# Performance work log

Hardware: AMD Instinct MI355X
Metric: run time of the kernel (lower is better)

## Reference

```python
import jax, jax.numpy as jnp
import numpy as np

N_HARM_XYZ = 6
N_HARM_DIR = 4
HIDDEN_XYZ = 256
HIDDEN_DIR = 128
EMB_XYZ = N_HARM_XYZ * 2 * 3 + 3  # 39
EMB_DIR = N_HARM_DIR * 2 * 3 + 3  # 27


def harmonic_embedding(x, n_harmonics):
    # x: [..., 3] -> [..., n_harmonics*2*3 + 3]
    freqs = 2.0 ** jnp.arange(n_harmonics, dtype=x.dtype)  # logspace, omega0=1
    emb = (x[..., None] * freqs).reshape(*x.shape[:-1], -1)  # [..., 3*n_harm]
    return jnp.concatenate([jnp.sin(emb), jnp.cos(emb), x], axis=-1)


def setup_inputs() -> dict:
    key = jax.random.key(0)
    ks = jax.random.split(key, 32)
    R, P = 2048, 64
    inp = {
        'sample_points': jax.random.normal(ks[0], (R, P, 3), dtype=jnp.float32),
        'directions': jax.random.normal(ks[1], (R, 3), dtype=jnp.float32),
    }
    # trunk layer dims (skip concat before layer 5; last layer outputs hidden+1)
    dims_in = [EMB_XYZ, HIDDEN_XYZ, HIDDEN_XYZ, HIDDEN_XYZ, HIDDEN_XYZ,
               HIDDEN_XYZ + EMB_XYZ, HIDDEN_XYZ, HIDDEN_XYZ]
    dims_out = [HIDDEN_XYZ] * 7 + [HIDDEN_XYZ + 1]
    for i, (di, do) in enumerate(zip(dims_in, dims_out)):
        s = 1.0 / np.sqrt(di)
        inp[f'W{i}'] = jax.random.uniform(ks[2 + 2 * i], (di, do), jnp.float32, -s, s)
        inp[f'b{i}'] = jax.random.uniform(ks[3 + 2 * i], (do,), jnp.float32, -s, s)
    s = 1.0 / np.sqrt(HIDDEN_XYZ + EMB_DIR)
    inp['Wc'] = jax.random.uniform(ks[20], (HIDDEN_XYZ + EMB_DIR, HIDDEN_DIR), jnp.float32, -s, s)
    inp['bc'] = jax.random.uniform(ks[21], (HIDDEN_DIR,), jnp.float32, -s, s)
    s = 1.0 / np.sqrt(HIDDEN_DIR)
    inp['Wo'] = jax.random.uniform(ks[22], (HIDDEN_DIR, 3), jnp.float32, -s, s)
    inp['bo'] = jax.random.uniform(ks[23], (3,), jnp.float32, -s, s)
    return inp


def nerf_forward(sample_points, directions,
                 W0, b0, W1, b1, W2, b2, W3, b3, W4, b4, W5, b5, W6, b6, W7, b7,
                 Wc, bc, Wo, bo):
    R, P, _ = sample_points.shape
    pts = sample_points.reshape(-1, 3)              # [N, 3]
    e = harmonic_embedding(pts, N_HARM_XYZ)         # [N, 39]
    h = e
    # seq0: layers 0-4, ReLU after each
    for W, b in ((W0, b0), (W1, b1), (W2, b2), (W3, b3), (W4, b4)):
        h = jax.nn.relu(h @ W + b)
    # skip concat with xyz embedding, then seq1: layers 5-7 (no ReLU after last)
    h = jnp.concatenate([h, e], axis=-1)            # [N, 295]
    h = jax.nn.relu(h @ W5 + b5)
    h = jax.nn.relu(h @ W6 + b6)
    h = h @ W7 + b7                                  # [N, 257]
    sigma = jax.nn.relu(h[:, 0]).reshape(R, P, 1)
    dirs = jnp.broadcast_to(directions[:, None, :], (R, P, 3)).reshape(-1, 3)
    d = harmonic_embedding(dirs, N_HARM_DIR)         # [N, 27]
    c = jnp.concatenate([h[:, 1:], d], axis=-1)      # [N, 283]
    c = jax.nn.relu(c @ Wc + bc)
    color = jax.nn.sigmoid(c @ Wo + bo).reshape(R, P, 3)
    return color, sigma


def reference(sample_points, directions,
              W0, b0, W1, b1, W2, b2, W3, b3, W4, b4, W5, b5, W6, b6, W7, b7,
              Wc, bc, Wo, bo):
    # returns (feature, density) matching the torch dict values
    return nerf_forward(sample_points, directions,
                        W0, b0, W1, b1, W2, b2, W3, b3, W4, b4, W5, b5, W6, b6, W7, b7,
                        Wc, bc, Wo, bo)
```

## Files before the change

kernel.cpp:

```cpp
#include <hip/hip_runtime.h>

typedef __attribute__((ext_vector_type(8))) __bf16 bf16x8;
typedef __attribute__((ext_vector_type(4))) float float4_;
typedef __attribute__((ext_vector_type(4))) unsigned short ushort4_;

#define ACT_STRIDE 264
#define EMB_STRIDE 72

#define OFF_W0T 0
#define OFF_W1T 16384
#define OFF_W2T 81920
#define OFF_W3T 147456
#define OFF_W4T 212992
#define OFF_W5T 278528
#define OFF_W6T 360448
#define OFF_W7T 425984
#define OFF_WCT 491520
#define BF16_TOTAL 524288
#define WSF_BYTE_OFF (BF16_TOTAL * 2)

__device__ __forceinline__ unsigned short f2b(float v) {
  union { float f; unsigned u; } a; a.f = v;
  unsigned r = a.u + 0x7fffu + ((a.u >> 16) & 1u);
  return (unsigned short)(r >> 16);
}
__device__ __forceinline__ float b2f(unsigned short h) {
  union { unsigned u; float f; } a; a.u = ((unsigned)h) << 16;
  return a.f;
}

__global__ __launch_bounds__(256) void prep_kernel(
    const float* __restrict__ W0, const float* __restrict__ W1,
    const float* __restrict__ W2, const float* __restrict__ W3,
    const float* __restrict__ W4, const float* __restrict__ W5,
    const float* __restrict__ W6, const float* __restrict__ W7,
    const float* __restrict__ Wc, const float* __restrict__ b7,
    unsigned short* __restrict__ wsb, float* __restrict__ wsf)
{
  int i = blockIdx.x * 256 + threadIdx.x;
  const float* src; int rs, K, Kp, n, k2; unsigned short* base;
  if (i < 8192)        { int t = i;          n = t & 255; k2 = t >> 8; src = W0; rs = 256; K = 39;  Kp = 64;  base = wsb + OFF_W0T; }
  else if (i < 139264) { int t = i - 8192;   int l = t >> 15; t &= 32767;
                         n = t & 255; k2 = t >> 8;
                         src = (l == 0) ? W1 : (l == 1) ? W2 : (l == 2) ? W3 : W4;
                         rs = 256; K = 256; Kp = 256; base = wsb + OFF_W1T + l * 65536; }
  else if (i < 180224) { int t = i - 139264; n = t & 255; k2 = t >> 8; src = W5;     rs = 256; K = 295; Kp = 320; base = wsb + OFF_W5T; }
  else if (i < 212992) { int t = i - 180224; n = t & 255; k2 = t >> 8; src = W6;     rs = 256; K = 256; Kp = 256; base = wsb + OFF_W6T; }
  else if (i < 245760) { int t = i - 212992; n = t & 255; k2 = t >> 8; src = W7 + 1; rs = 257; K = 256; Kp = 256; base = wsb + OFF_W7T; }
  else if (i < 262144) { int t = i - 245760; n = t & 127; k2 = t >> 7; src = Wc;     rs = 128; K = 256; Kp = 256; base = wsb + OFF_WCT; }
  else if (i < 262400) { int k = i - 262144; wsf[k] = W7[k * 257]; return; }
  else if (i < 262656) { int k = i - 262400; wsf[256 + k] = b7[k + 1]; return; }
  else return;
  const int k = k2 * 2;
  const float v0 = (k     < K) ? src[k * rs + n]       : 0.f;
  const float v1 = (k + 1 < K) ? src[(k + 1) * rs + n] : 0.f;
  const int off = (((n >> 4) * (Kp >> 5)) + (k >> 5)) * 512
                + ((k >> 3) & 3) * 128 + (n & 15) * 8 + (k & 7);
  const unsigned val = (unsigned)f2b(v0) | ((unsigned)f2b(v1) << 16);
  *(unsigned*)(base + off) = val;
}

template<bool RELU>
__device__ __forceinline__ void layer_mm(
    const unsigned short* src1, int stride1, int ks1,
    const unsigned short* src2, int stride2, int ks2,
    const unsigned short* __restrict__ wT, int kTiles,
    const float* bias, unsigned short* dst, int lane, int wave)
{
  const int c = lane & 15, q = lane >> 4;
  const int nt0 = wave * 2, n0 = wave * 32;
  float4_ acc[4][2] = {};

#pragma unroll
  for (int ks = 0; ks < 8; ++ks) {
    if (ks >= ks1) break;
    bf16x8 bfr[4];
    const unsigned short* p = src1 + c * stride1 + ks * 32 + q * 8;
#pragma unroll
    for (int mi = 0; mi < 4; ++mi)
      bfr[mi] = *(const bf16x8*)(p + mi * 16 * stride1);
#pragma unroll
    for (int ni = 0; ni < 2; ++ni) {
      bf16x8 afr = *(const bf16x8*)(wT + ((nt0 + ni) * kTiles + ks) * 512 + lane * 8);
#pragma unroll
      for (int mi = 0; mi < 4; ++mi)
        acc[mi][ni] = __builtin_amdgcn_mfma_f32_16x16x32_bf16(afr, bfr[mi], acc[mi][ni], 0, 0, 0);
    }
  }
#pragma unroll
  for (int ks = 0; ks < 2; ++ks) {
    if (ks >= ks2) break;
    bf16x8 bfr[4];
    const unsigned short* p = src2 + c * stride2 + ks * 32 + q * 8;
#pragma unroll
    for (int mi = 0; mi < 4; ++mi)
      bfr[mi] = *(const bf16x8*)(p + mi * 16 * stride2);
#pragma unroll
    for (int ni = 0; ni < 2; ++ni) {
      bf16x8 afr = *(const bf16x8*)(wT + ((nt0 + ni) * kTiles + ks1 + ks) * 512 + lane * 8);
#pragma unroll
      for (int mi = 0; mi < 4; ++mi)
        acc[mi][ni] = __builtin_amdgcn_mfma_f32_16x16x32_bf16(afr, bfr[mi], acc[mi][ni], 0, 0, 0);
    }
  }
#pragma unroll
  for (int ni = 0; ni < 2; ++ni) {
    const int n = n0 + ni * 16 + q * 4;
    float4_ bv = *(const float4_*)(bias + n);
#pragma unroll
    for (int mi = 0; mi < 4; ++mi) {
      float4_ v = acc[mi][ni] + bv;
      if (RELU) {
        v.x = fmaxf(v.x, 0.f); v.y = fmaxf(v.y, 0.f);
        v.z = fmaxf(v.z, 0.f); v.w = fmaxf(v.w, 0.f);
      }
      ushort4_ pk = { f2b(v.x), f2b(v.y), f2b(v.z), f2b(v.w) };
      *(ushort4_*)(dst + (mi * 16 + c) * ACT_STRIDE + n) = pk;
    }
  }
}

__global__ __launch_bounds__(512, 4) void nerf_kernel(
    const float* __restrict__ pts, const float* __restrict__ dirs,
    const float* __restrict__ b0, const float* __restrict__ b1,
    const float* __restrict__ b2, const float* __restrict__ b3,
    const float* __restrict__ b4, const float* __restrict__ b5,
    const float* __restrict__ b6, const float* __restrict__ b7,
    const float* __restrict__ Wc, const float* __restrict__ bc,
    const float* __restrict__ Wo, const float* __restrict__ bo,
    const unsigned short* __restrict__ wsb, const float* __restrict__ wsf,
    float* __restrict__ out)
{
  __shared__ __align__(16) unsigned short sA[64 * ACT_STRIDE];
  __shared__ __align__(16) unsigned short sB[64 * ACT_STRIDE];
  __shared__ __align__(16) unsigned short sE[64 * EMB_STRIDE];
  __shared__ float s_dvec[27];
  __shared__ float s_biasc[128];

  const int ray = blockIdx.x;
  const int t = threadIdx.x;
  const int lane = t & 63;
  const int wave = t >> 6;

  {
    const int m = t >> 3, s8 = t & 7;
    const float* pb = pts + (ray * 64 + m) * 3;
    const float x0 = pb[0], x1 = pb[1], x2 = pb[2];
#pragma unroll
    for (int j = 0; j < 9; ++j) {
      const int cc = s8 * 9 + j;
      float v = 0.f;
      if (cc < 18) {
        const float xx = (cc < 6) ? x0 : (cc < 12) ? x1 : x2;
        v = sinf(xx * (float)(1 << (cc % 6)));
      } else if (cc < 36) {
        const int c2 = cc - 18;
        const float xx = (c2 < 6) ? x0 : (c2 < 12) ? x1 : x2;
        v = cosf(xx * (float)(1 << (c2 % 6)));
      } else if (cc == 36) v = x0;
      else if (cc == 37) v = x1;
      else if (cc == 38) v = x2;
      sE[m * EMB_STRIDE + cc] = f2b(v);
    }
  }
  if (t < 27) {
    const float* db = dirs + ray * 3;
    float v;
    if (t < 12) v = sinf(db[t >> 2] * (float)(1 << (t & 3)));
    else if (t < 24) { const int j = t - 12; v = cosf(db[j >> 2] * (float)(1 << (j & 3))); }
    else v = db[t - 24];
    s_dvec[t] = v;
  }
  __syncthreads();
  if (t < 128) {
    float s = bc[t];
#pragma unroll
    for (int j = 0; j < 27; ++j) s += s_dvec[j] * Wc[(256 + j) * 128 + t];
    s_biasc[t] = s;
  }

  layer_mm<true >(sE, EMB_STRIDE, 2, nullptr, 0, 0, wsb + OFF_W0T, 2,  b0, sA, lane, wave); __syncthreads();
  layer_mm<true >(sA, ACT_STRIDE, 8, nullptr, 0, 0, wsb + OFF_W1T, 8,  b1, sB, lane, wave); __syncthreads();
  layer_mm<true >(sB, ACT_STRIDE, 8, nullptr, 0, 0, wsb + OFF_W2T, 8,  b2, sA, lane, wave); __syncthreads();
  layer_mm<true >(sA, ACT_STRIDE, 8, nullptr, 0, 0, wsb + OFF_W3T, 8,  b3, sB, lane, wave); __syncthreads();
  layer_mm<true >(sB, ACT_STRIDE, 8, nullptr, 0, 0, wsb + OFF_W4T, 8,  b4, sA, lane, wave); __syncthreads();
  layer_mm<true >(sA, ACT_STRIDE, 8, sE, EMB_STRIDE, 2, wsb + OFF_W5T, 10, b5, sB, lane, wave); __syncthreads();
  layer_mm<true >(sB, ACT_STRIDE, 8, nullptr, 0, 0, wsb + OFF_W6T, 8,  b6, sA, lane, wave); __syncthreads();

  {
    const int m = t >> 3, q8 = t & 7;
    const unsigned short* p = sA + m * ACT_STRIDE + q8 * 32;
    const float* w = wsf + q8 * 32;
    float s = 0.f;
#pragma unroll
    for (int i = 0; i < 4; ++i) {
      bf16x8 hv = *(const bf16x8*)(p + i * 8);
#pragma unroll
      for (int j = 0; j < 8; ++j) s += (float)hv[j] * w[i * 8 + j];
    }
    s += __shfl_xor(s, 1); s += __shfl_xor(s, 2); s += __shfl_xor(s, 4);
    if (q8 == 0) out[393216 + ray * 64 + m] = fmaxf(s + b7[0], 0.f);
  }

  layer_mm<false>(sA, ACT_STRIDE, 8, nullptr, 0, 0, wsb + OFF_W7T, 8, wsf + 256, sB, lane, wave); __syncthreads();
  if (wave < 4)
    layer_mm<true>(sB, ACT_STRIDE, 8, nullptr, 0, 0, wsb + OFF_WCT, 8, s_biasc, sA, lane, wave);
  __syncthreads();

  {
    const int m = t >> 3, q8 = t & 7;
    const unsigned short* p = sA + m * ACT_STRIDE + q8 * 16;
    float s0 = 0.f, s1 = 0.f, s2 = 0.f;
#pragma unroll
    for (int i = 0; i < 2; ++i) {
      bf16x8 cv = *(const bf16x8*)(p + i * 8);
#pragma unroll
      for (int j = 0; j < 8; ++j) {
        const float cc = (float)cv[j];
        const float* w = Wo + (q8 * 16 + i * 8 + j) * 3;
        s0 += cc * w[0]; s1 += cc * w[1]; s2 += cc * w[2];
      }
    }
    s0 += __shfl_xor(s0, 1); s0 += __shfl_xor(s0, 2); s0 += __shfl_xor(s0, 4);
    s1 += __shfl_xor(s1, 1); s1 += __shfl_xor(s1, 2); s1 += __shfl_xor(s1, 4);
    s2 += __shfl_xor(s2, 1); s2 += __shfl_xor(s2, 2); s2 += __shfl_xor(s2, 4);
    if (q8 == 0) {
      float* oc = out + (ray * 64 + m) * 3;
      oc[0] = 1.f / (1.f + __expf(-(s0 + bo[0])));
      oc[1] = 1.f / (1.f + __expf(-(s1 + bo[1])));
      oc[2] = 1.f / (1.f + __expf(-(s2 + bo[2])));
    }
  }
}

extern "C" void kernel_launch(void* const* d_in, const int* in_sizes, int n_in,
                              void* d_out, int out_size, void* d_ws, size_t ws_size,
                              hipStream_t stream)
{
  const float* pts  = (const float*)d_in[0];
  const float* dirs = (const float*)d_in[1];
  const float* W0 = (const float*)d_in[2];   const float* b0 = (const float*)d_in[3];
  const float* W1 = (const float*)d_in[4];   const float* b1 = (const float*)d_in[5];
  const float* W2 = (const float*)d_in[6];   const float* b2 = (const float*)d_in[7];
  const float* W3 = (const float*)d_in[8];   const float* b3 = (const float*)d_in[9];
  const float* W4 = (const float*)d_in[10];  const float* b4 = (const float*)d_in[11];
  const float* W5 = (const float*)d_in[12];  const float* b5 = (const float*)d_in[13];
  const float* W6 = (const float*)d_in[14];  const float* b6 = (const float*)d_in[15];
  const float* W7 = (const float*)d_in[16];  const float* b7 = (const float*)d_in[17];
  const float* Wc = (const float*)d_in[18];  const float* bc = (const float*)d_in[19];
  const float* Wo = (const float*)d_in[20];  const float* bo = (const float*)d_in[21];

  unsigned short* wsb = (unsigned short*)d_ws;
  float* wsf = (float*)((char*)d_ws + WSF_BYTE_OFF);

  prep_kernel<<<1026, 256, 0, stream>>>(W0, W1, W2, W3, W4, W5, W6, W7, Wc, b7, wsb, wsf);
  nerf_kernel<<<2048, 512, 0, stream>>>(pts, dirs, b0, b1, b2, b3, b4, b5, b6, b7,
                                        Wc, bc, Wo, bo, wsb, wsf, (float*)d_out);
}
```

Baseline: 257.8 us.

## Store activations in MFMA fragment-tiled LDS layout and template layer K-steps

```diff
diff --git a/kernel.cpp b/kernel.cpp
--- a/kernel.cpp
+++ b/kernel.cpp
@@ -3,9 +3,7 @@
 typedef __attribute__((ext_vector_type(8))) __bf16 bf16x8;
 typedef __attribute__((ext_vector_type(4))) float float4_;
 typedef __attribute__((ext_vector_type(4))) unsigned short ushort4_;
-
-#define ACT_STRIDE 264
-#define EMB_STRIDE 72
+typedef __attribute__((ext_vector_type(8))) unsigned short ushort8_;
 
 #define OFF_W0T 0
 #define OFF_W1T 16384
@@ -23,10 +21,6 @@
   union { float f; unsigned u; } a; a.f = v;
   unsigned r = a.u + 0x7fffu + ((a.u >> 16) & 1u);
   return (unsigned short)(r >> 16);
-}
-__device__ __forceinline__ float b2f(unsigned short h) {
-  union { unsigned u; float f; } a; a.u = ((unsigned)h) << 16;
-  return a.f;
 }
 
 __global__ __launch_bounds__(256) void prep_kernel(
@@ -60,44 +54,40 @@
   *(unsigned*)(base + off) = val;
 }
 
-template<bool RELU>
+template<int KS1, int KS2, bool RELU>
 __device__ __forceinline__ void layer_mm(
-    const unsigned short* src1, int stride1, int ks1,
-    const unsigned short* src2, int stride2, int ks2,
-    const unsigned short* __restrict__ wT, int kTiles,
+    const unsigned short* src1, const unsigned short* src2,
+    const unsigned short* __restrict__ wT,
     const float* bias, unsigned short* dst, int lane, int wave)
 {
+  constexpr int KT = KS1 + KS2;
   const int c = lane & 15, q = lane >> 4;
   const int nt0 = wave * 2, n0 = wave * 32;
   float4_ acc[4][2] = {};
 
 #pragma unroll
-  for (int ks = 0; ks < 8; ++ks) {
-    if (ks >= ks1) break;
+  for (int ks = 0; ks < KS1; ++ks) {
     bf16x8 bfr[4];
-    const unsigned short* p = src1 + c * stride1 + ks * 32 + q * 8;
 #pragma unroll
     for (int mi = 0; mi < 4; ++mi)
-      bfr[mi] = *(const bf16x8*)(p + mi * 16 * stride1);
+      bfr[mi] = *(const bf16x8*)(src1 + (ks * 4 + mi) * 512 + lane * 8);
 #pragma unroll
     for (int ni = 0; ni < 2; ++ni) {
-      bf16x8 afr = *(const bf16x8*)(wT + ((nt0 + ni) * kTiles + ks) * 512 + lane * 8);
+      bf16x8 afr = *(const bf16x8*)(wT + ((nt0 + ni) * KT + ks) * 512 + lane * 8);
 #pragma unroll
       for (int mi = 0; mi < 4; ++mi)
         acc[mi][ni] = __builtin_amdgcn_mfma_f32_16x16x32_bf16(afr, bfr[mi], acc[mi][ni], 0, 0, 0);
     }
   }
 #pragma unroll
-  for (int ks = 0; ks < 2; ++ks) {
-    if (ks >= ks2) break;
+  for (int ks = 0; ks < KS2; ++ks) {
     bf16x8 bfr[4];
-    const unsigned short* p = src2 + c * stride2 + ks * 32 + q * 8;
 #pragma unroll
     for (int mi = 0; mi < 4; ++mi)
-      bfr[mi] = *(const bf16x8*)(p + mi * 16 * stride2);
+      bfr[mi] = *(const bf16x8*)(src2 + (ks * 4 + mi) * 512 + lane * 8);
 #pragma unroll
     for (int ni = 0; ni < 2; ++ni) {
-      bf16x8 afr = *(const bf16x8*)(wT + ((nt0 + ni) * kTiles + ks1 + ks) * 512 + lane * 8);
+      bf16x8 afr = *(const bf16x8*)(wT + ((nt0 + ni) * KT + KS1 + ks) * 512 + lane * 8);
 #pragma unroll
       for (int mi = 0; mi < 4; ++mi)
         acc[mi][ni] = __builtin_amdgcn_mfma_f32_16x16x32_bf16(afr, bfr[mi], acc[mi][ni], 0, 0, 0);
@@ -105,8 +95,8 @@
   }
 #pragma unroll
   for (int ni = 0; ni < 2; ++ni) {
-    const int n = n0 + ni * 16 + q * 4;
-    float4_ bv = *(const float4_*)(bias + n);
+    const int base = n0 + ni * 16 + q * 4;
+    float4_ bv = *(const float4_*)(bias + base);
 #pragma unroll
     for (int mi = 0; mi < 4; ++mi) {
       float4_ v = acc[mi][ni] + bv;
@@ -115,7 +105,9 @@
         v.z = fmaxf(v.z, 0.f); v.w = fmaxf(v.w, 0.f);
       }
       ushort4_ pk = { f2b(v.x), f2b(v.y), f2b(v.z), f2b(v.w) };
-      *(ushort4_*)(dst + (mi * 16 + c) * ACT_STRIDE + n) = pk;
+      const int addr = ((base >> 5) * 4 + mi) * 512
+                     + ((base >> 3) & 3) * 128 + c * 8 + (base & 7);
+      *(ushort4_*)(dst + addr) = pk;
     }
   }
 }
@@ -131,9 +123,8 @@
     const unsigned short* __restrict__ wsb, const float* __restrict__ wsf,
     float* __restrict__ out)
 {
-  __shared__ __align__(16) unsigned short sA[64 * ACT_STRIDE];
-  __shared__ __align__(16) unsigned short sB[64 * ACT_STRIDE];
-  __shared__ __align__(16) unsigned short sE[64 * EMB_STRIDE];
+  __shared__ __align__(16) unsigned short sA[32 * 512];
+  __shared__ __align__(16) unsigned short sB[40 * 512];
   __shared__ float s_dvec[27];
   __shared__ float s_biasc[128];
 
@@ -141,14 +132,16 @@
   const int t = threadIdx.x;
   const int lane = t & 63;
   const int wave = t >> 6;
+  unsigned short* sE = sB + 32 * 512;
 
   {
     const int m = t >> 3, s8 = t & 7;
     const float* pb = pts + (ray * 64 + m) * 3;
     const float x0 = pb[0], x1 = pb[1], x2 = pb[2];
-#pragma unroll
-    for (int j = 0; j < 9; ++j) {
-      const int cc = s8 * 9 + j;
+    ushort8_ ev;
+#pragma unroll
+    for (int j = 0; j < 8; ++j) {
+      const int cc = s8 * 8 + j;
       float v = 0.f;
       if (cc < 18) {
         const float xx = (cc < 6) ? x0 : (cc < 12) ? x1 : x2;
@@ -160,8 +153,9 @@
       } else if (cc == 36) v = x0;
       else if (cc == 37) v = x1;
       else if (cc == 38) v = x2;
-      sE[m * EMB_STRIDE + cc] = f2b(v);
-    }
+      ev[j] = f2b(v);
+    }
+    *(ushort8_*)(sE + ((s8 >> 2) * 4 + (m >> 4)) * 512 + (s8 & 3) * 128 + (m & 15) * 8) = ev;
   }
   if (t < 27) {
     const float* db = dirs + ray * 3;
@@ -179,45 +173,46 @@
     s_biasc[t] = s;
   }
 
-  layer_mm<true >(sE, EMB_STRIDE, 2, nullptr, 0, 0, wsb + OFF_W0T, 2,  b0, sA, lane, wave); __syncthreads();
-  layer_mm<true >(sA, ACT_STRIDE, 8, nullptr, 0, 0, wsb + OFF_W1T, 8,  b1, sB, lane, wave); __syncthreads();
-  layer_mm<true >(sB, ACT_STRIDE, 8, nullptr, 0, 0, wsb + OFF_W2T, 8,  b2, sA, lane, wave); __syncthreads();
-  layer_mm<true >(sA, ACT_STRIDE, 8, nullptr, 0, 0, wsb + OFF_W3T, 8,  b3, sB, lane, wave); __syncthreads();
-  layer_mm<true >(sB, ACT_STRIDE, 8, nullptr, 0, 0, wsb + OFF_W4T, 8,  b4, sA, lane, wave); __syncthreads();
-  layer_mm<true >(sA, ACT_STRIDE, 8, sE, EMB_STRIDE, 2, wsb + OFF_W5T, 10, b5, sB, lane, wave); __syncthreads();
-  layer_mm<true >(sB, ACT_STRIDE, 8, nullptr, 0, 0, wsb + OFF_W6T, 8,  b6, sA, lane, wave); __syncthreads();
+  layer_mm<2, 0, true >(sE, nullptr, wsb + OFF_W0T, b0, sA, lane, wave); __syncthreads();
+  layer_mm<8, 0, true >(sA, nullptr, wsb + OFF_W1T, b1, sB, lane, wave); __syncthreads();
+  layer_mm<8, 0, true >(sB, nullptr, wsb + OFF_W2T, b2, sA, lane, wave); __syncthreads();
+  layer_mm<8, 0, true >(sA, nullptr, wsb + OFF_W3T, b3, sB, lane, wave); __syncthreads();
+  layer_mm<8, 0, true >(sB, nullptr, wsb + OFF_W4T, b4, sA, lane, wave); __syncthreads();
+  layer_mm<8, 2, true >(sA, sE,      wsb + OFF_W5T, b5, sB, lane, wave); __syncthreads();
+  layer_mm<8, 0, true >(sB, nullptr, wsb + OFF_W6T, b6, sA, lane, wave); __syncthreads();
 
   {
     const int m = t >> 3, q8 = t & 7;
-    const unsigned short* p = sA + m * ACT_STRIDE + q8 * 32;
+    const unsigned short* pbase = sA + (q8 * 4 + (m >> 4)) * 512 + (m & 15) * 8;
     const float* w = wsf + q8 * 32;
     float s = 0.f;
 #pragma unroll
-    for (int i = 0; i < 4; ++i) {
-      bf16x8 hv = *(const bf16x8*)(p + i * 8);
-#pragma unroll
-      for (int j = 0; j < 8; ++j) s += (float)hv[j] * w[i * 8 + j];
+    for (int i8 = 0; i8 < 4; ++i8) {
+      bf16x8 hv = *(const bf16x8*)(pbase + i8 * 128);
+#pragma unroll
+      for (int j = 0; j < 8; ++j) s += (float)hv[j] * w[i8 * 8 + j];
     }
     s += __shfl_xor(s, 1); s += __shfl_xor(s, 2); s += __shfl_xor(s, 4);
     if (q8 == 0) out[393216 + ray * 64 + m] = fmaxf(s + b7[0], 0.f);
   }
 
-  layer_mm<false>(sA, ACT_STRIDE, 8, nullptr, 0, 0, wsb + OFF_W7T, 8, wsf + 256, sB, lane, wave); __syncthreads();
+  layer_mm<8, 0, false>(sA, nullptr, wsb + OFF_W7T, wsf + 256, sB, lane, wave); __syncthreads();
   if (wave < 4)
-    layer_mm<true>(sB, ACT_STRIDE, 8, nullptr, 0, 0, wsb + OFF_WCT, 8, s_biasc, sA, lane, wave);
+    layer_mm<8, 0, true>(sB, nullptr, wsb + OFF_WCT, s_biasc, sA, lane, wave);
   __syncthreads();
 
   {
     const int m = t >> 3, q8 = t & 7;
-    const unsigned short* p = sA + m * ACT_STRIDE + q8 * 16;
     float s0 = 0.f, s1 = 0.f, s2 = 0.f;
 #pragma unroll
-    for (int i = 0; i < 2; ++i) {
-      bf16x8 cv = *(const bf16x8*)(p + i * 8);
+    for (int i2 = 0; i2 < 2; ++i2) {
+      const int kb = q8 * 16 + i2 * 8;
+      bf16x8 cv = *(const bf16x8*)(sA + ((kb >> 5) * 4 + (m >> 4)) * 512
+                                      + ((kb >> 3) & 3) * 128 + (m & 15) * 8);
 #pragma unroll
       for (int j = 0; j < 8; ++j) {
         const float cc = (float)cv[j];
-        const float* w = Wo + (q8 * 16 + i * 8 + j) * 3;
+        const float* w = Wo + (kb + j) * 3;
         s0 += cc * w[0]; s1 += cc * w[1]; s2 += cc * w[2];
       }
     }
```

Result: no change. 255.2 us (-1.0%).
